# Kernel optimization log

Hardware: AMD Instinct MI355X
Metric: run time of the kernel (lower is better)

## Reference

```python
import jax, jax.numpy as jnp
import numpy as np

N_QUBITS = 6
N_LAYERS = 3
DIM = 2 ** N_QUBITS  # 64
BATCH = 262144
FEATURE_DIM = 4
HIDDEN_DIM = 16
N_CLASSES = 4
N_QW = N_LAYERS * N_QUBITS * 3  # 54


def _apply_1q(state, gate, q):
    """Apply a single-qubit gate to qubit q (little-endian: qubit 0 = LSB).
    state: [B, DIM] complex64. gate: [2,2] (shared) or [B,2,2] (per-sample)."""
    B = state.shape[0]
    st = state.reshape(B, 2 ** (N_QUBITS - 1 - q), 2, 2 ** q)
    if gate.ndim == 2:
        out = jnp.einsum('ij,bkjl->bkil', gate, st)
    else:
        out = jnp.einsum('bij,bkjl->bkil', gate, st)
    return out.reshape(B, DIM)


def _cx_perm(c, t):
    # CX(control=c, target=t) is a permutation of basis states: flip bit t where bit c is 1.
    idx = np.arange(DIM)
    return jnp.asarray(idx ^ (((idx >> c) & 1) << t))


def _ry_batched(theta):  # theta: [B] -> [B,2,2]
    c = jnp.cos(theta / 2).astype(jnp.complex64)
    s = jnp.sin(theta / 2).astype(jnp.complex64)
    return jnp.stack([jnp.stack([c, -s], -1), jnp.stack([s, c], -1)], -2)


def _rx(t):  # scalar angle -> [2,2]
    c = jnp.cos(t / 2).astype(jnp.complex64)
    s = jnp.sin(t / 2).astype(jnp.complex64)
    return jnp.stack([jnp.stack([c, -1j * s]), jnp.stack([-1j * s, c])]).astype(jnp.complex64)


def _ry(t):
    c = jnp.cos(t / 2).astype(jnp.complex64)
    s = jnp.sin(t / 2).astype(jnp.complex64)
    return jnp.stack([jnp.stack([c, -s]), jnp.stack([s, c])]).astype(jnp.complex64)


def _rz(t):
    e_m = jnp.exp(-0.5j * t).astype(jnp.complex64)
    e_p = jnp.exp(0.5j * t).astype(jnp.complex64)
    z = jnp.zeros((), jnp.complex64)
    return jnp.stack([jnp.stack([e_m, z]), jnp.stack([z, e_p])])


_H = (jnp.array([[1, 1], [1, -1]], jnp.float32) / np.float32(np.sqrt(2.0))).astype(jnp.complex64)
# signs[s, q] = +1 if bit q of basis state s is 0, else -1  -> Z expectation via probs @ signs
_SIGNS = jnp.asarray(
    1.0 - 2.0 * ((np.arange(DIM)[:, None] >> np.arange(N_QUBITS)[None, :]) & 1),
    dtype=jnp.float32)


def quantum_expectations(angles, qw):
    """Exact batched statevector simulation of the parameterized circuit.
    angles: [B, N_QUBITS] input-encoding RY angles; qw: [N_QW] variational params.
    Returns per-qubit Z expectations [B, N_QUBITS] (exact, i.e. infinite-shot limit)."""
    B = angles.shape[0]
    state = jnp.zeros((B, DIM), jnp.complex64).at[:, 0].set(1.0)
    # Encoding: H then RY(x_q) on each qubit
    for q in range(N_QUBITS):
        state = _apply_1q(state, _H, q)
        state = _apply_1q(state, _ry_batched(angles[:, q]), q)
    # Variational layers
    p = 0
    for _layer in range(N_LAYERS):
        for q in range(N_QUBITS - 1):
            state = state[:, _cx_perm(q, q + 1)]
        for q in range(N_QUBITS):
            state = _apply_1q(state, _rx(qw[p]), q); p += 1
            state = _apply_1q(state, _ry(qw[p]), q); p += 1
            state = _apply_1q(state, _rz(qw[p]), q); p += 1
    probs = state.real ** 2 + state.imag ** 2  # [B, DIM]
    return probs @ _SIGNS  # [B, N_QUBITS]


def setup_inputs() -> dict:
    key = jax.random.key(0)
    ks = jax.random.split(key, 10)
    d = {
        'x': jax.random.normal(ks[0], (BATCH, FEATURE_DIM), jnp.float32),
        'pre_w1': jax.random.normal(ks[1], (FEATURE_DIM, HIDDEN_DIM), jnp.float32) * 0.3,
        'pre_b1': jnp.zeros((HIDDEN_DIM,), jnp.float32),
        'pre_w2': jax.random.normal(ks[2], (HIDDEN_DIM, N_QUBITS), jnp.float32) * 0.2,
        'pre_b2': jnp.zeros((N_QUBITS,), jnp.float32),
        'qw': jax.random.normal(ks[3], (N_QW,), jnp.float32) * 0.1,
        'post_w1': jax.random.normal(ks[4], (N_QUBITS, HIDDEN_DIM), jnp.float32) * 0.3,
        'post_b1': jnp.zeros((HIDDEN_DIM,), jnp.float32),
        'post_w2': jax.random.normal(ks[5], (HIDDEN_DIM, N_CLASSES), jnp.float32) * 0.2,
        'post_b2': jnp.zeros((N_CLASSES,), jnp.float32),
    }
    return d


def reference(x, pre_w1, pre_b1, pre_w2, pre_b2, qw, post_w1, post_b1, post_w2, post_b2):
    # classical_preprocess (dropout is identity in eval): Linear -> ReLU -> Linear -> Tanh
    h = jax.nn.relu(x @ pre_w1 + pre_b1)
    angles = jnp.tanh(h @ pre_w2 + pre_b2)  # [B, N_QUBITS]
    # quantum circuit (original detaches inputs before the circuit -> no grad through it)
    exp = jax.lax.stop_gradient(quantum_expectations(angles, qw))
    # classical_postprocess: Linear -> ReLU -> Linear
    h2 = jax.nn.relu(exp @ post_w1 + post_b1)
    return h2 @ post_w2 + post_b2
```

## Files before the change

kernel.cpp:

```cpp
#include <hip/hip_runtime.h>
#include <math.h>

#define NQ 6
#define NLAYERS 3
#define QBATCH 262144
#define NGATES 18
#define GSTRIDE 40

typedef float  f2  __attribute__((ext_vector_type(2)));
typedef float  f4v __attribute__((ext_vector_type(4)));
typedef __fp16 h2v __attribute__((ext_vector_type(2)));
typedef __fp16 h8v __attribute__((ext_vector_type(8)));

__device__ __forceinline__ float lane_swap(float v) {
    return __int_as_float(__builtin_amdgcn_update_dpp(
        0, __float_as_int(v), 0xB1, 0xF, 0xF, true));
}
__device__ __forceinline__ f2 lane_swap2(f2 v) {
    f2 r; r.x = lane_swap(v.x); r.y = lane_swap(v.y); return r;
}
__device__ __forceinline__ float tanh_fast(float a) {
    const float e = __expf(2.f * a);
    return 1.f - 2.f * __builtin_amdgcn_rcpf(e + 1.f);
}

__global__ __launch_bounds__(128) void prep_kernel(
    const float* __restrict__ qw,
    const float* __restrict__ post_w1,
    __fp16* __restrict__ wfrag)
{
    __shared__ f2    gs2[NGATES * GSTRIDE / 2];
    __shared__ float Ure[64][65];
    __shared__ float Uim[64][65];
    const int tid = threadIdx.x;

    if (tid < NGATES) {
        const int pp = tid * 3;
        float s0 = sinf(qw[pp+0]*0.5f), c0 = cosf(qw[pp+0]*0.5f);
        float s1 = sinf(qw[pp+1]*0.5f), c1 = cosf(qw[pp+1]*0.5f);
        float s2 = sinf(qw[pp+2]*0.5f), c2 = cosf(qw[pp+2]*0.5f);
        const float m00r =  c1*c0, m00i =  s1*s0;
        const float m01r = -s1*c0, m01i = -c1*s0;
        const float m10r =  s1*c0, m10i = -c1*s0;
        const float m11r =  c1*c0, m11i = -s1*s0;
        const float g00r = c2*m00r + s2*m00i, g00i = c2*m00i - s2*m00r;
        const float g01r = c2*m01r + s2*m01i, g01i = c2*m01i - s2*m01r;
        const float g10r = c2*m10r - s2*m10i, g10i = c2*m10i + s2*m10r;
        const float g11r = c2*m11r - s2*m11i, g11i = c2*m11i + s2*m11r;
        float* o = (float*)gs2 + tid * GSTRIDE;
        o[0]=o[1]=g00r;  o[2]=o[3]=g00i;  o[4]=o[5]=-g00i;
        o[6]=o[7]=g01r;  o[8]=o[9]=g01i;  o[10]=o[11]=-g01i;
        o[12]=o[13]=g10r; o[14]=o[15]=g10i; o[16]=o[17]=-g10i;
        o[18]=o[19]=g11r; o[20]=o[21]=g11i; o[22]=o[23]=-g11i;
        o[24]=g00r; o[25]=g10r;  o[26]=g00i; o[27]=g10i;
        o[28]=-g00i; o[29]=-g10i; o[30]=g01r; o[31]=g11r;
        o[32]=g01i; o[33]=g11i;  o[34]=-g01i; o[35]=-g11i;
        o[36]=o[37]=o[38]=o[39]=0.f;
    }
    __syncthreads();

    {
        const int bt = tid >> 1, p = tid & 1;
        f2 R[16], U[16];
        #pragma unroll
        for (int j = 0; j < 16; ++j) {
            R[j].x = ((bt >> 5) == p && (bt & 31) == 2*j    ) ? 1.f : 0.f;
            R[j].y = ((bt >> 5) == p && (bt & 31) == 2*j + 1) ? 1.f : 0.f;
            U[j].x = 0.f; U[j].y = 0.f;
        }
        const f2* gpack = gs2;
        #pragma unroll 1
        for (int l = 0; l < NLAYERS; ++l) {
            #pragma unroll
            for (int j = 0; j < 16; j += 2) {
                float t;
                t = R[j].y; R[j].y = R[j+1].y; R[j+1].y = t;
                t = U[j].y; U[j].y = U[j+1].y; U[j+1].y = t;
            }
            #pragma unroll
            for (int c = 1; c < 4; ++c) {
                #pragma unroll
                for (int j = 0; j < 16; ++j) {
                    if (((j >> (c-1)) & 1) && !((j >> c) & 1)) {
                        const int t = j | (1 << c);
                        f2 tmp;
                        tmp = R[j]; R[j] = R[t]; R[t] = tmp;
                        tmp = U[j]; U[j] = U[t]; U[t] = tmp;
                    }
                }
            }
            #pragma unroll
            for (int j = 8; j < 16; ++j) {
                R[j] = lane_swap2(R[j]);
                U[j] = lane_swap2(U[j]);
            }
            const f2* lg = gpack + l * (NQ * (GSTRIDE / 2));
            {
                const f2* gb = lg;
                const f2 A = gb[12], Ai = gb[13], nAi = gb[14];
                const f2 C = gb[15], Ci = gb[16], nCi = gb[17];
                #pragma unroll
                for (int j = 0; j < 16; ++j) {
                    const f2 z = R[j], u = U[j];
                    const f2 br0 = __builtin_shufflevector(z, z, 0, 0);
                    const f2 br1 = __builtin_shufflevector(z, z, 1, 1);
                    const f2 bu0 = __builtin_shufflevector(u, u, 0, 0);
                    const f2 bu1 = __builtin_shufflevector(u, u, 1, 1);
                    R[j] = __builtin_elementwise_fma(nCi, bu1, __builtin_elementwise_fma(C,  br1, __builtin_elementwise_fma(nAi, bu0, A  * br0)));
                    U[j] = __builtin_elementwise_fma(C,   bu1, __builtin_elementwise_fma(Ci, br1, __builtin_elementwise_fma(A,   bu0, Ai * br0)));
                }
            }
            #pragma unroll
            for (int q = 1; q < 5; ++q) {
                const f2* gb = lg + q * (GSTRIDE / 2);
                const f2 a00r = gb[0], a00i = gb[1],  n00i = gb[2];
                const f2 a01r = gb[3], a01i = gb[4],  n01i = gb[5];
                const f2 a10r = gb[6], a10i = gb[7],  n10i = gb[8];
                const f2 a11r = gb[9], a11i = gb[10], n11i = gb[11];
                const int bit = 1 << (q - 1);
                #pragma unroll
                for (int m = 0; m < 8; ++m) {
                    const int ja = ((m >> (q-1)) << q) | (m & (bit - 1));
                    const int jb = ja | bit;
                    const f2 zr0 = R[ja], zu0 = U[ja];
                    const f2 zr1 = R[jb], zu1 = U[jb];
                    R[ja] = __builtin_elementwise_fma(n01i, zu1, __builtin_elementwise_fma(a01r, zr1, __builtin_elementwise_fma(n00i, zu0, a00r * zr0)));
                    U[ja] = __builtin_elementwise_fma(a01r, zu1, __builtin_elementwise_fma(a01i, zr1, __builtin_elementwise_fma(a00r, zu0, a00i * zr0)));
                    R[jb] = __builtin_elementwise_fma(n11i, zu1, __builtin_elementwise_fma(a11r, zr1, __builtin_elementwise_fma(n10i, zu0, a10r * zr0)));
                    U[jb] = __builtin_elementwise_fma(a11r, zu1, __builtin_elementwise_fma(a11i, zr1, __builtin_elementwise_fma(a10r, zu0, a10i * zr0)));
                }
            }
            {
                const f2* gb = lg + 5 * (GSTRIDE / 2);
                const bool sw = (p != 0);
                const f2 rrr  = sw ? gb[9]  : gb[0];
                const f2 rri  = sw ? gb[10] : gb[1];
                const f2 nrri = sw ? gb[11] : gb[2];
                const f2 rpr  = sw ? gb[6]  : gb[3];
                const f2 rpi  = sw ? gb[7]  : gb[4];
                const f2 nrpi = sw ? gb[8]  : gb[5];
                #pragma unroll
                for (int j = 0; j < 16; ++j) {
                    const f2 z = R[j], u = U[j];
                    const f2 pr = lane_swap2(z), pu = lane_swap2(u);
                    R[j] = __builtin_elementwise_fma(nrpi, pu, __builtin_elementwise_fma(rpr, pr, __builtin_elementwise_fma(nrri, u, rrr * z)));
                    U[j] = __builtin_elementwise_fma(rpr,  pu, __builtin_elementwise_fma(rpi, pr, __builtin_elementwise_fma(rrr,  u, rri * z)));
                }
            }
        }
        #pragma unroll
        for (int j = 0; j < 16; ++j) {
            Ure[32*p + 2*j    ][bt] = R[j].x;
            Ure[32*p + 2*j + 1][bt] = R[j].y;
            Uim[32*p + 2*j    ][bt] = U[j].x;
            Uim[32*p + 2*j + 1][bt] = U[j].y;
        }
    }
    __syncthreads();

    if (tid < 64) {
        const int rlow = tid & 15, kg = tid >> 4;
        for (int f = 0; f < 16; ++f) {
            const int otile = f >> 1, ks = f & 1;
            const int row = 16*otile + rlow;
            const int n = row >> 1, cmp = row & 1;
            h8v v;
            #pragma unroll
            for (int e = 0; e < 8; ++e) {
                const int k = kg*8 + e + 32*ks;
                v[e] = (__fp16)(cmp ? Uim[n][k] : Ure[n][k]);
            }
            *(h8v*)(wfrag + f*512 + tid*8) = v;
        }
        float cw[6];
        #pragma unroll
        for (int q = 0; q < 6; ++q) cw[q] = post_w1[q*16 + rlow];
        for (int f = 0; f < 2; ++f) {
            h8v v;
            #pragma unroll
            for (int e = 0; e < 8; ++e) {
                const int k2 = kg*8 + e + 32*f;
                float s = 0.f;
                #pragma unroll
                for (int q = 0; q < 6; ++q)
                    s += ((k2 >> q) & 1) ? -cw[q] : cw[q];
                v[e] = (__fp16)s;
            }
            *(h8v*)(wfrag + 8192 + f*512 + tid*8) = v;
        }
    }
}

__global__ __launch_bounds__(256) void qnn_mfma_kernel(
    const float* __restrict__ x,
    const float* __restrict__ pre_w1, const float* __restrict__ pre_b1,
    const float* __restrict__ pre_w2, const float* __restrict__ pre_b2,
    const __fp16* __restrict__ wfrag,
    const float* __restrict__ post_b1, const float* __restrict__ post_w2,
    const float* __restrict__ post_b2,
    float* __restrict__ out)
{
    __shared__ __align__(16) __fp16 w1s[8192];
    __shared__ __align__(16) __fp16 ps[4][1024];
    const int tid = threadIdx.x;
    {
        const uint4* src = (const uint4*)wfrag;
        uint4* dst = (uint4*)w1s;
        #pragma unroll
        for (int i = 0; i < 4; ++i) dst[tid + i*256] = src[tid + i*256];
    }
    __syncthreads();

    const int lane = tid & 63, wid = tid >> 6;
    const int sbase = (blockIdx.x * 4 + wid) * 64;

    const h8v a2f0 = *(const h8v*)(wfrag + 8192 + lane*8);
    const h8v a2f1 = *(const h8v*)(wfrag + 8192 + 512 + lane*8);

    const float4 xv = ((const float4*)x)[sbase + lane];
    float h[16];
    #pragma unroll
    for (int j = 0; j < 16; ++j) {
        float a = pre_b1[j];
        a = fmaf(xv.x, pre_w1[0*16+j], a);
        a = fmaf(xv.y, pre_w1[1*16+j], a);
        a = fmaf(xv.z, pre_w1[2*16+j], a);
        a = fmaf(xv.w, pre_w1[3*16+j], a);
        h[j] = fmaxf(a, 0.f);
    }
    float fc[NQ], fs[NQ];
    #pragma unroll
    for (int q = 0; q < NQ; ++q) {
        float a = pre_b2[q];
        #pragma unroll
        for (int j = 0; j < 16; ++j) a = fmaf(h[j], pre_w2[j*NQ+q], a);
        const float y = 0.5f * tanh_fast(a) + 0.78539816339744831f;
        fc[q] = __cosf(y); fs[q] = __sinf(y);
    }
    const float b2x = post_b2[0], b2y = post_b2[1];
    const float b2z = post_b2[2], b2w = post_b2[3];

    const int sl = lane & 15, g = lane >> 4;
    const int swz = (sl & 7) << 4;
    __fp16* myp = ps[wid];

    #pragma unroll
    for (int G = 0; G < 4; ++G) {
        const int srcb = (G * 16 + sl) << 2;
        #define BP(v) __int_as_float(__builtin_amdgcn_ds_bpermute(srcb, __float_as_int(v)))
        const float q0c=BP(fc[0]), q0s=BP(fs[0]);
        const float q1c=BP(fc[1]), q1s=BP(fs[1]);
        const float q2c=BP(fc[2]), q2s=BP(fs[2]);
        const float q3c=BP(fc[3]), q3s=BP(fs[3]);
        const float q4c=BP(fc[4]), q4s=BP(fs[4]);
        const float q5c=BP(fc[5]), q5s=BP(fs[5]);
        #undef BP
        const float f3  = (g & 1) ? q3s : q3c;
        const float f4  = (g & 2) ? q4s : q4c;
        const float f34 = f3 * f4;
        const float pre0 = f34 * q5c, pre1 = f34 * q5s;
        float t01[4], b8[8];
        t01[0] = q0c*q1c; t01[1] = q0s*q1c; t01[2] = q0c*q1s; t01[3] = q0s*q1s;
        #pragma unroll
        for (int e = 0; e < 8; ++e) b8[e] = t01[e & 3] * ((e & 4) ? q2s : q2c);
        h8v bf0, bf1;
        #pragma unroll
        for (int e2 = 0; e2 < 4; ++e2) {
            const h2v t0 = __builtin_amdgcn_cvt_pkrtz(b8[2*e2]*pre0, b8[2*e2+1]*pre0);
            const h2v t1 = __builtin_amdgcn_cvt_pkrtz(b8[2*e2]*pre1, b8[2*e2+1]*pre1);
            bf0[2*e2] = t0[0]; bf0[2*e2+1] = t0[1];
            bf1[2*e2] = t1[0]; bf1[2*e2+1] = t1[1];
        }

        f4v acc[8];
        #pragma unroll
        for (int t = 0; t < 8; ++t) {
            const h8v a0 = *(const h8v*)(w1s + (t*2+0)*512 + lane*8);
            const h8v a1 = *(const h8v*)(w1s + (t*2+1)*512 + lane*8);
            f4v z = {0.f, 0.f, 0.f, 0.f};
            z = __builtin_amdgcn_mfma_f32_16x16x32_f16(a0, bf0, z, 0, 0, 0);
            acc[t] = __builtin_amdgcn_mfma_f32_16x16x32_f16(a1, bf1, z, 0, 0, 0);
        }
        #pragma unroll
        for (int t = 0; t < 8; ++t) {
            const float p0 = fmaf(acc[t].x, acc[t].x, acc[t].y * acc[t].y);
            const float p1 = fmaf(acc[t].z, acc[t].z, acc[t].w * acc[t].w);
            const h2v ph = __builtin_amdgcn_cvt_pkrtz(p0, p1);
            *(h2v*)((char*)myp + sl*128 + ((16*t + 4*g) ^ swz)) = ph;
        }
        const h8v pb0 = *(const h8v*)((const char*)myp + sl*128 + ((16*g     ) ^ swz));
        const h8v pb1 = *(const h8v*)((const char*)myp + sl*128 + ((16*g + 64) ^ swz));
        f4v c2 = {0.f, 0.f, 0.f, 0.f};
        c2 = __builtin_amdgcn_mfma_f32_16x16x32_f16(a2f0, pb0, c2, 0, 0, 0);
        c2 = __builtin_amdgcn_mfma_f32_16x16x32_f16(a2f1, pb1, c2, 0, 0, 0);

        const float4 b1v = ((const float4*)post_b1)[g];
        const float e0  = fmaxf(c2.x + b1v.x, 0.f);
        const float e1  = fmaxf(c2.y + b1v.y, 0.f);
        const float e2_ = fmaxf(c2.z + b1v.z, 0.f);
        const float e3  = fmaxf(c2.w + b1v.w, 0.f);
        const float4 w0 = ((const float4*)post_w2)[4*g + 0];
        const float4 w1 = ((const float4*)post_w2)[4*g + 1];
        const float4 w2 = ((const float4*)post_w2)[4*g + 2];
        const float4 w3 = ((const float4*)post_w2)[4*g + 3];
        float ox = fmaf(e0, w0.x, fmaf(e1, w1.x, fmaf(e2_, w2.x, e3 * w3.x)));
        float oy = fmaf(e0, w0.y, fmaf(e1, w1.y, fmaf(e2_, w2.y, e3 * w3.y)));
        float oz = fmaf(e0, w0.z, fmaf(e1, w1.z, fmaf(e2_, w2.z, e3 * w3.z)));
        float ow = fmaf(e0, w0.w, fmaf(e1, w1.w, fmaf(e2_, w2.w, e3 * w3.w)));
        ox += __shfl_xor(ox, 16, 64); ox += __shfl_xor(ox, 32, 64);
        oy += __shfl_xor(oy, 16, 64); oy += __shfl_xor(oy, 32, 64);
        oz += __shfl_xor(oz, 16, 64); oz += __shfl_xor(oz, 32, 64);
        ow += __shfl_xor(ow, 16, 64); ow += __shfl_xor(ow, 32, 64);
        if (lane < 16) {
            float4 r;
            r.x = ox + b2x; r.y = oy + b2y; r.z = oz + b2z; r.w = ow + b2w;
            ((float4*)out)[sbase + G*16 + sl] = r;
        }
    }
}

extern "C" void kernel_launch(void* const* d_in, const int* in_sizes, int n_in,
                              void* d_out, int out_size, void* d_ws, size_t ws_size,
                              hipStream_t stream) {
    const float* x       = (const float*)d_in[0];
    const float* pre_w1  = (const float*)d_in[1];
    const float* pre_b1  = (const float*)d_in[2];
    const float* pre_w2  = (const float*)d_in[3];
    const float* pre_b2  = (const float*)d_in[4];
    const float* qw      = (const float*)d_in[5];
    const float* post_w1 = (const float*)d_in[6];
    const float* post_b1 = (const float*)d_in[7];
    const float* post_w2 = (const float*)d_in[8];
    const float* post_b2 = (const float*)d_in[9];
    float* out = (float*)d_out;
    __fp16* wfrag = (__fp16*)d_ws;

    prep_kernel<<<1, 128, 0, stream>>>(qw, post_w1, wfrag);
    qnn_mfma_kernel<<<QBATCH / 256, 256, 0, stream>>>(
        x, pre_w1, pre_b1, pre_w2, pre_b2, wfrag,
        post_b1, post_w2, post_b2, out);
}
```

Before: 26.15 us.

## Switch circuit matmul to 32x32x16 MFMA with register-resident weight fragments

Reorganizes the 64x128 unitary fragments for 32x32x16 MFMA tiles and has each wave load all 16 fragments directly into registers. This removes the shared-memory staging of the weight matrix and the block barrier. Each loop iteration now covers 32 samples instead of 16, so fewer bpermutes and MFMA issues are needed per sample. The prep kernel is rewritten to emit the new fragment layout using two waves. The cost is much higher VGPR pressure (16 h8v fragments plus 4 sixteen-wide accumulators), which may lower occupancy.

Result: faster. 25.53 us (-2.4%).

```diff
diff --git a/kernel.cpp b/kernel.cpp
--- a/kernel.cpp
+++ b/kernel.cpp
@@ -7,10 +7,11 @@
 #define NGATES 18
 #define GSTRIDE 40
 
-typedef float  f2  __attribute__((ext_vector_type(2)));
-typedef float  f4v __attribute__((ext_vector_type(4)));
-typedef __fp16 h2v __attribute__((ext_vector_type(2)));
-typedef __fp16 h8v __attribute__((ext_vector_type(8)));
+typedef float  f2   __attribute__((ext_vector_type(2)));
+typedef float  f4v  __attribute__((ext_vector_type(4)));
+typedef float  f16f __attribute__((ext_vector_type(16)));
+typedef __fp16 h2v  __attribute__((ext_vector_type(2)));
+typedef __fp16 h8v  __attribute__((ext_vector_type(8)));
 
 __device__ __forceinline__ float lane_swap(float v) {
     return __int_as_float(__builtin_amdgcn_update_dpp(
@@ -158,35 +159,36 @@
     }
     __syncthreads();
 
-    if (tid < 64) {
-        const int rlow = tid & 15, kg = tid >> 4;
-        for (int f = 0; f < 16; ++f) {
-            const int otile = f >> 1, ks = f & 1;
-            const int row = 16*otile + rlow;
-            const int n = row >> 1, cmp = row & 1;
+    {
+        const int lane = tid & 63, w = tid >> 6;
+        const int r32 = lane & 31, kh = lane >> 5;
+        for (int i = w; i < 16; i += 2) {
+            const int T = i >> 2, s = i & 3;
+            const int row = 32*T + r32, n = row >> 1, cmp = row & 1;
+            const float* src = cmp ? &Uim[n][0] : &Ure[n][0];
             h8v v;
             #pragma unroll
-            for (int e = 0; e < 8; ++e) {
-                const int k = kg*8 + e + 32*ks;
-                v[e] = (__fp16)(cmp ? Uim[n][k] : Ure[n][k]);
-            }
-            *(h8v*)(wfrag + f*512 + tid*8) = v;
-        }
-        float cw[6];
-        #pragma unroll
-        for (int q = 0; q < 6; ++q) cw[q] = post_w1[q*16 + rlow];
-        for (int f = 0; f < 2; ++f) {
-            h8v v;
-            #pragma unroll
-            for (int e = 0; e < 8; ++e) {
-                const int k2 = kg*8 + e + 32*f;
-                float s = 0.f;
-                #pragma unroll
-                for (int q = 0; q < 6; ++q)
-                    s += ((k2 >> q) & 1) ? -cw[q] : cw[q];
-                v[e] = (__fp16)s;
-            }
-            *(h8v*)(wfrag + 8192 + f*512 + tid*8) = v;
+            for (int e = 0; e < 8; ++e) v[e] = (__fp16)src[kh*8 + 16*s + e];
+            *(h8v*)(wfrag + i*512 + lane*8) = v;
+        }
+        if (w == 0) {
+            const int rlow = lane & 15, kg = lane >> 4;
+            float cw[6];
+            #pragma unroll
+            for (int q = 0; q < 6; ++q) cw[q] = post_w1[q*16 + rlow];
+            for (int f = 0; f < 2; ++f) {
+                h8v v;
+                #pragma unroll
+                for (int e = 0; e < 8; ++e) {
+                    const int k2 = kg*8 + e + 32*f;
+                    float sacc = 0.f;
+                    #pragma unroll
+                    for (int q = 0; q < 6; ++q)
+                        sacc += ((k2 >> q) & 1) ? -cw[q] : cw[q];
+                    v[e] = (__fp16)sacc;
+                }
+                *(h8v*)(wfrag + 8192 + f*512 + lane*8) = v;
+            }
         }
     }
 }
@@ -200,20 +202,15 @@
     const float* __restrict__ post_b2,
     float* __restrict__ out)
 {
-    __shared__ __align__(16) __fp16 w1s[8192];
-    __shared__ __align__(16) __fp16 ps[4][1024];
-    const int tid = threadIdx.x;
-    {
-        const uint4* src = (const uint4*)wfrag;
-        uint4* dst = (uint4*)w1s;
-        #pragma unroll
-        for (int i = 0; i < 4; ++i) dst[tid + i*256] = src[tid + i*256];
-    }
-    __syncthreads();
-
+    __shared__ __align__(16) __fp16 ps[4][2048];
+    const int tid  = threadIdx.x;
     const int lane = tid & 63, wid = tid >> 6;
     const int sbase = (blockIdx.x * 4 + wid) * 64;
 
+    h8v a1f[16];
+    #pragma unroll
+    for (int i = 0; i < 16; ++i)
+        a1f[i] = *(const h8v*)(wfrag + i*512 + lane*8);
     const h8v a2f0 = *(const h8v*)(wfrag + 8192 + lane*8);
     const h8v a2f1 = *(const h8v*)(wfrag + 8192 + 512 + lane*8);
 
@@ -240,13 +237,14 @@
     const float b2x = post_b2[0], b2y = post_b2[1];
     const float b2z = post_b2[2], b2w = post_b2[3];
 
-    const int sl = lane & 15, g = lane >> 4;
-    const int swz = (sl & 7) << 4;
+    const int sl32 = lane & 31, kh = lane >> 5;
+    const int sl16 = lane & 15, g2 = lane >> 4;
     __fp16* myp = ps[wid];
+    const int wswz = (sl32 & 7) << 4;
 
     #pragma unroll
-    for (int G = 0; G < 4; ++G) {
-        const int srcb = (G * 16 + sl) << 2;
+    for (int G2 = 0; G2 < 2; ++G2) {
+        const int srcb = (G2 * 32 + sl32) << 2;
         #define BP(v) __int_as_float(__builtin_amdgcn_ds_bpermute(srcb, __float_as_int(v)))
         const float q0c=BP(fc[0]), q0s=BP(fs[0]);
         const float q1c=BP(fc[1]), q1s=BP(fs[1]);
@@ -255,66 +253,79 @@
         const float q4c=BP(fc[4]), q4s=BP(fs[4]);
         const float q5c=BP(fc[5]), q5s=BP(fs[5]);
         #undef BP
-        const float f3  = (g & 1) ? q3s : q3c;
-        const float f4  = (g & 2) ? q4s : q4c;
-        const float f34 = f3 * f4;
-        const float pre0 = f34 * q5c, pre1 = f34 * q5s;
+        const float f3v = kh ? q3s : q3c;
         float t01[4], b8[8];
         t01[0] = q0c*q1c; t01[1] = q0s*q1c; t01[2] = q0c*q1s; t01[3] = q0s*q1s;
         #pragma unroll
         for (int e = 0; e < 8; ++e) b8[e] = t01[e & 3] * ((e & 4) ? q2s : q2c);
-        h8v bf0, bf1;
-        #pragma unroll
-        for (int e2 = 0; e2 < 4; ++e2) {
-            const h2v t0 = __builtin_amdgcn_cvt_pkrtz(b8[2*e2]*pre0, b8[2*e2+1]*pre0);
-            const h2v t1 = __builtin_amdgcn_cvt_pkrtz(b8[2*e2]*pre1, b8[2*e2+1]*pre1);
-            bf0[2*e2] = t0[0]; bf0[2*e2+1] = t0[1];
-            bf1[2*e2] = t1[0]; bf1[2*e2+1] = t1[1];
-        }
-
-        f4v acc[8];
-        #pragma unroll
-        for (int t = 0; t < 8; ++t) {
-            const h8v a0 = *(const h8v*)(w1s + (t*2+0)*512 + lane*8);
-            const h8v a1 = *(const h8v*)(w1s + (t*2+1)*512 + lane*8);
-            f4v z = {0.f, 0.f, 0.f, 0.f};
-            z = __builtin_amdgcn_mfma_f32_16x16x32_f16(a0, bf0, z, 0, 0, 0);
-            acc[t] = __builtin_amdgcn_mfma_f32_16x16x32_f16(a1, bf1, z, 0, 0, 0);
-        }
-        #pragma unroll
-        for (int t = 0; t < 8; ++t) {
-            const float p0 = fmaf(acc[t].x, acc[t].x, acc[t].y * acc[t].y);
-            const float p1 = fmaf(acc[t].z, acc[t].z, acc[t].w * acc[t].w);
-            const h2v ph = __builtin_amdgcn_cvt_pkrtz(p0, p1);
-            *(h2v*)((char*)myp + sl*128 + ((16*t + 4*g) ^ swz)) = ph;
-        }
-        const h8v pb0 = *(const h8v*)((const char*)myp + sl*128 + ((16*g     ) ^ swz));
-        const h8v pb1 = *(const h8v*)((const char*)myp + sl*128 + ((16*g + 64) ^ swz));
-        f4v c2 = {0.f, 0.f, 0.f, 0.f};
-        c2 = __builtin_amdgcn_mfma_f32_16x16x32_f16(a2f0, pb0, c2, 0, 0, 0);
-        c2 = __builtin_amdgcn_mfma_f32_16x16x32_f16(a2f1, pb1, c2, 0, 0, 0);
-
-        const float4 b1v = ((const float4*)post_b1)[g];
-        const float e0  = fmaxf(c2.x + b1v.x, 0.f);
-        const float e1  = fmaxf(c2.y + b1v.y, 0.f);
-        const float e2_ = fmaxf(c2.z + b1v.z, 0.f);
-        const float e3  = fmaxf(c2.w + b1v.w, 0.f);
-        const float4 w0 = ((const float4*)post_w2)[4*g + 0];
-        const float4 w1 = ((const float4*)post_w2)[4*g + 1];
-        const float4 w2 = ((const float4*)post_w2)[4*g + 2];
-        const float4 w3 = ((const float4*)post_w2)[4*g + 3];
-        float ox = fmaf(e0, w0.x, fmaf(e1, w1.x, fmaf(e2_, w2.x, e3 * w3.x)));
-        float oy = fmaf(e0, w0.y, fmaf(e1, w1.y, fmaf(e2_, w2.y, e3 * w3.y)));
-        float oz = fmaf(e0, w0.z, fmaf(e1, w1.z, fmaf(e2_, w2.z, e3 * w3.z)));
-        float ow = fmaf(e0, w0.w, fmaf(e1, w1.w, fmaf(e2_, w2.w, e3 * w3.w)));
-        ox += __shfl_xor(ox, 16, 64); ox += __shfl_xor(ox, 32, 64);
-        oy += __shfl_xor(oy, 16, 64); oy += __shfl_xor(oy, 32, 64);
-        oz += __shfl_xor(oz, 16, 64); oz += __shfl_xor(oz, 32, 64);
-        ow += __shfl_xor(ow, 16, 64); ow += __shfl_xor(ow, 32, 64);
-        if (lane < 16) {
-            float4 r;
-            r.x = ox + b2x; r.y = oy + b2y; r.z = oz + b2z; r.w = ow + b2w;
-            ((float4*)out)[sbase + G*16 + sl] = r;
+        h8v bs[4];
+        #pragma unroll
+        for (int s = 0; s < 4; ++s) {
+            const float pre = f3v * ((s & 1) ? q4s : q4c) * ((s & 2) ? q5s : q5c);
+            #pragma unroll
+            for (int e2 = 0; e2 < 4; ++e2) {
+                const h2v t = __builtin_amdgcn_cvt_pkrtz(b8[2*e2]*pre, b8[2*e2+1]*pre);
+                bs[s][2*e2] = t[0]; bs[s][2*e2+1] = t[1];
+            }
+        }
+
+        f16f acc[4];
+        #pragma unroll
+        for (int T = 0; T < 4; ++T) acc[T] = (f16f)(0.f);
+        #pragma unroll
+        for (int s = 0; s < 4; ++s) {
+            #pragma unroll
+            for (int T = 0; T < 4; ++T)
+                acc[T] = __builtin_amdgcn_mfma_f32_32x32x16_f16(
+                    a1f[T*4 + s], bs[s], acc[T], 0, 0, 0);
+        }
+
+        #pragma unroll
+        for (int T = 0; T < 4; ++T) {
+            #pragma unroll
+            for (int a = 0; a < 4; ++a) {
+                const float p0 = fmaf(acc[T][4*a+0], acc[T][4*a+0],
+                                      acc[T][4*a+1] * acc[T][4*a+1]);
+                const float p1 = fmaf(acc[T][4*a+2], acc[T][4*a+2],
+                                      acc[T][4*a+3] * acc[T][4*a+3]);
+                const h2v ph = __builtin_amdgcn_cvt_pkrtz(p0, p1);
+                const int boff = (32*T + 8*a + 4*kh) ^ wswz;
+                *(h2v*)((char*)myp + sl32*128 + boff) = ph;
+            }
+        }
+
+        #pragma unroll
+        for (int H = 0; H < 2; ++H) {
+            const int smp  = H*16 + sl16;
+            const int rswz = (smp & 7) << 4;
+            const h8v pb0 = *(const h8v*)((const char*)myp + smp*128 + ((16*g2     ) ^ rswz));
+            const h8v pb1 = *(const h8v*)((const char*)myp + smp*128 + ((16*g2 + 64) ^ rswz));
+            f4v c2 = {0.f, 0.f, 0.f, 0.f};
+            c2 = __builtin_amdgcn_mfma_f32_16x16x32_f16(a2f0, pb0, c2, 0, 0, 0);
+            c2 = __builtin_amdgcn_mfma_f32_16x16x32_f16(a2f1, pb1, c2, 0, 0, 0);
+
+            const float4 b1v = ((const float4*)post_b1)[g2];
+            const float e0  = fmaxf(c2.x + b1v.x, 0.f);
+            const float e1  = fmaxf(c2.y + b1v.y, 0.f);
+            const float e2_ = fmaxf(c2.z + b1v.z, 0.f);
+            const float e3  = fmaxf(c2.w + b1v.w, 0.f);
+            const float4 w0 = ((const float4*)post_w2)[4*g2 + 0];
+            const float4 w1 = ((const float4*)post_w2)[4*g2 + 1];
+            const float4 w2 = ((const float4*)post_w2)[4*g2 + 2];
+            const float4 w3 = ((const float4*)post_w2)[4*g2 + 3];
+            float ox = fmaf(e0, w0.x, fmaf(e1, w1.x, fmaf(e2_, w2.x, e3 * w3.x)));
+            float oy = fmaf(e0, w0.y, fmaf(e1, w1.y, fmaf(e2_, w2.y, e3 * w3.y)));
+            float oz = fmaf(e0, w0.z, fmaf(e1, w1.z, fmaf(e2_, w2.z, e3 * w3.z)));
+            float ow = fmaf(e0, w0.w, fmaf(e1, w1.w, fmaf(e2_, w2.w, e3 * w3.w)));
+            ox += __shfl_xor(ox, 16, 64); ox += __shfl_xor(ox, 32, 64);
+            oy += __shfl_xor(oy, 16, 64); oy += __shfl_xor(oy, 32, 64);
+            oz += __shfl_xor(oz, 16, 64); oz += __shfl_xor(oz, 32, 64);
+            ow += __shfl_xor(ow, 16, 64); ow += __shfl_xor(ow, 32, 64);
+            if (lane < 16) {
+                float4 r;
+                r.x = ox + b2x; r.y = oy + b2y; r.z = oz + b2z; r.w = ow + b2w;
+                ((float4*)out)[sbase + G2*32 + H*16 + sl16] = r;
+            }
         }
     }
 }
```
